# Kernel tuning notes

Hardware: AMD Instinct MI355X
Metric: run time of the kernel (lower is better)

Reference implementation:

```python
import jax, jax.numpy as jnp
import numpy as np
import math

EPS = 1.1920929e-07  # torch F.rms_norm default eps = fp32 machine epsilon


def rms_norm(x):
    # normalize over last dim, no learned weight (matches F.rms_norm(x, (d,)))
    var = jnp.mean(jnp.square(x), axis=-1, keepdims=True)
    return x * jax.lax.rsqrt(var + EPS)


def rotary(x, cos, sin):
    # x: (B, T, H, D); cos/sin: (T, D) -> broadcast over B, H
    d2 = x.shape[-1] // 2
    x1, x2 = x[..., :d2], x[..., d2:]
    rot = jnp.concatenate([-x2, x1], axis=-1)  # rotate_half
    c = cos[None, :, None, :]
    s = sin[None, :, None, :]
    return x * c + rot * s


def setup_inputs() -> dict:
    key = jax.random.key(0)
    ks = jax.random.split(key, 5)
    B, T, C, H = 2, 2048, 1024, 16
    D = C // H
    x = jax.random.normal(ks[0], (B, T, C), dtype=jnp.float32)
    # real RoPE tables (theta=10000), duplicated across the two halves
    inv_freq = 1.0 / (10000.0 ** (np.arange(0, D, 2, dtype=np.float32) / D))
    pos = np.arange(T, dtype=np.float32)
    freqs = np.outer(pos, inv_freq)            # (T, D/2)
    emb = np.concatenate([freqs, freqs], -1)   # (T, D)
    cos = jnp.asarray(np.cos(emb), dtype=jnp.float32)
    sin = jnp.asarray(np.sin(emb), dtype=jnp.float32)
    sc_in = 1.0 / math.sqrt(C)
    W_attn = jax.random.normal(ks[1], (C, 3 * C), dtype=jnp.float32) * sc_in
    b_attn = jax.random.normal(ks[2], (3 * C,), dtype=jnp.float32) * 0.02
    W_proj = jax.random.normal(ks[3], (C, C), dtype=jnp.float32) * sc_in
    b_proj = jax.random.normal(ks[4], (C,), dtype=jnp.float32) * 0.02
    return {"x": x, "cos": cos, "sin": sin, "W_attn": W_attn, "b_attn": b_attn,
            "W_proj": W_proj, "b_proj": b_proj}


def reference(x, cos, sin, W_attn, b_attn, W_proj, b_proj):
    B, T, C = x.shape
    H = 16
    D = C // H
    qkv = x @ W_attn + b_attn                         # (B, T, 3C)
    qkv = qkv.reshape(B, T, 3, H, D)                  # 'b t (a h d) -> ...'
    q, k, v = qkv[:, :, 0], qkv[:, :, 1], qkv[:, :, 2]  # (B, T, H, D)
    q, k = rms_norm(q), rms_norm(k)
    q = rotary(q, cos, sin)
    k = rotary(k, cos, sin)
    # causal SDPA, scale = 1/sqrt(D)
    scale = 1.0 / math.sqrt(D)
    scores = jnp.einsum('bthd,bshd->bhts', q, k) * scale  # (B, H, T, T)
    causal = jnp.tril(jnp.ones((T, T), dtype=bool))
    scores = jnp.where(causal[None, None], scores, jnp.finfo(scores.dtype).min)
    attn = jax.nn.softmax(scores, axis=-1)
    y = jnp.einsum('bhts,bshd->bthd', attn, v)            # (B, T, H, D)
    y = y.reshape(B, T, C)
    return y @ W_proj + b_proj
```

## Files before the change

### kernel.cpp

```cpp
#include <hip/hip_runtime.h>
#include <math.h>

#define EPSV 1.1920929e-07f

typedef __attribute__((ext_vector_type(8))) short short8;
typedef __attribute__((ext_vector_type(4))) float f32x4;

__device__ __forceinline__ float bf2f(unsigned short u) {
    union { unsigned int i; float f; } c; c.i = ((unsigned int)u) << 16; return c.f;
}
__device__ __forceinline__ unsigned short f2bf(float f) {
    union { float f; unsigned int i; } c; c.f = f;
    unsigned int r = c.i + 0x7FFFu + ((c.i >> 16) & 1u);
    return (unsigned short)(r >> 16);
}
__device__ __forceinline__ unsigned int pack_bf16_ru(float a, float b) {
    union { float f; unsigned int i; } ca, cb; ca.f = a; cb.f = b;
    return __builtin_amdgcn_perm(cb.i + 0x8000u, ca.i + 0x8000u, 0x07060302u);
}
__device__ __forceinline__ void async_lds16(const unsigned short* g, unsigned short* l) {
    __builtin_amdgcn_global_load_lds(
        (const __attribute__((address_space(1))) unsigned int*)g,
        (__attribute__((address_space(3))) unsigned int*)l, 16, 0, 0);
}

__global__ __launch_bounds__(256) void prep_cast_transpose(
    const float* __restrict__ x, unsigned short* __restrict__ xb, int nCast,
    const float* __restrict__ Wa, unsigned short* __restrict__ Wat,
    const float* __restrict__ Wp, unsigned short* __restrict__ Wpt,
    const float* __restrict__ cosp, const float* __restrict__ sinp,
    float2* __restrict__ cs, int castBlocks)
{
    __shared__ float tile[32][33];
    const int bxg = blockIdx.x;
    if (bxg < castBlocks) {
        const int i = (bxg * 256 + threadIdx.x) * 4;
        if (i >= nCast) return;
        const float4 v = *(const float4*)&x[i];
        ushort4 o;
        o.x = f2bf(v.x); o.y = f2bf(v.y); o.z = f2bf(v.z); o.w = f2bf(v.w);
        *(ushort4*)&xb[i] = o;
        return;
    }
    if (bxg >= castBlocks + 4096) {
        const int i = (bxg - castBlocks - 4096) * 256 + threadIdx.x;
        const int tp = i >> 5, dp = i & 31;
        cs[i] = make_float2(cosp[tp * 64 + dp], sinp[tp * 64 + dp]);
        return;
    }
    const int r0 = bxg - castBlocks;
    int bx = r0 & 127;
    const int by = r0 >> 7;
    const float* W; unsigned short* Wt; int N;
    if (bx < 96) { W = Wa; Wt = Wat; N = 3072; }
    else         { W = Wp; Wt = Wpt; N = 1024; bx -= 96; }
    const int n0 = bx * 32, k0 = by * 32;
    const int r = threadIdx.x >> 3, c4 = (threadIdx.x & 7) * 4;
    const float4 v = *(const float4*)&W[(size_t)(k0 + r) * N + n0 + c4];
    tile[r][c4 + 0] = v.x; tile[r][c4 + 1] = v.y;
    tile[r][c4 + 2] = v.z; tile[r][c4 + 3] = v.w;
    __syncthreads();
    ushort4 o;
    o.x = f2bf(tile[c4 + 0][r]); o.y = f2bf(tile[c4 + 1][r]);
    o.z = f2bf(tile[c4 + 2][r]); o.w = f2bf(tile[c4 + 3][r]);
    *(ushort4*)&Wt[(size_t)(n0 + r) * 1024 + k0 + c4] = o;
}

__global__ __launch_bounds__(256) void gemm_qkv(
    const unsigned short* __restrict__ A,
    const unsigned short* __restrict__ Bt,
    const float* __restrict__ bias,
    unsigned short* __restrict__ qkv,
    unsigned short* __restrict__ vt,
    const float2* __restrict__ cs,
    int M, int K, int T)
{
    const int N = 3072;
    __shared__ __align__(16) unsigned short smem[17408];
    unsigned short* As0 = smem;
    unsigned short* As1 = smem + 4096;
    unsigned short* Bs0 = smem + 8192;
    unsigned short* Bs1 = smem + 12288;

    const int t    = threadIdx.x;
    const int lane = t & 63;
    const int wv   = t >> 6;
    const int wrow = (wv >> 1) * 64;
    const int wcol = (wv & 1) * 64;
    const int m0 = blockIdx.y * 128;
    const int n0 = blockIdx.x * 128;
    const int col  = lane & 15;
    const int quad = lane >> 4;

    const int srow = (wv << 5) + (lane >> 2);
    const int scol = (lane & 3) << 3;
    const unsigned short* a00 = A  + (size_t)(m0 + srow) * K + scol;
    const unsigned short* a10 = a00 + (size_t)16 * K;
    const unsigned short* a01 = a00 + 32;
    const unsigned short* a11 = a10 + 32;
    const unsigned short* b00 = Bt + (size_t)(n0 + srow) * K + scol;
    const unsigned short* b10 = b00 + (size_t)16 * K;
    const unsigned short* b01 = b00 + 32;
    const unsigned short* b11 = b10 + 32;
    unsigned short* al0 = &As0[srow * 32 + scol];
    unsigned short* al1 = &As0[(srow + 16) * 32 + scol];
    unsigned short* al2 = &As1[srow * 32 + scol];
    unsigned short* al3 = &As1[(srow + 16) * 32 + scol];
    unsigned short* bl0 = &Bs0[srow * 32 + scol];
    unsigned short* bl1 = &Bs0[(srow + 16) * 32 + scol];
    unsigned short* bl2 = &Bs1[srow * 32 + scol];
    unsigned short* bl3 = &Bs1[(srow + 16) * 32 + scol];

    f32x4 acc[4][4];
    #pragma unroll
    for (int i = 0; i < 4; ++i)
        #pragma unroll
        for (int j = 0; j < 4; ++j)
            acc[i][j] = (f32x4){0.f, 0.f, 0.f, 0.f};

    for (int k0 = 0; k0 < K; k0 += 64) {
        async_lds16(a00, al0);
        async_lds16(a10, al1);
        async_lds16(a01, al2);
        async_lds16(a11, al3);
        async_lds16(b00, bl0);
        async_lds16(b10, bl1);
        async_lds16(b01, bl2);
        async_lds16(b11, bl3);
        a00 += 64; a10 += 64; a01 += 64; a11 += 64;
        b00 += 64; b10 += 64; b01 += 64; b11 += 64;
        __syncthreads();
        short8 af[2][4], bf[2][4];
        #pragma unroll
        for (int mt = 0; mt < 4; ++mt) {
            af[0][mt] = *(const short8*)&As0[(wrow + mt * 16 + col) * 32 + (quad << 3)];
            af[1][mt] = *(const short8*)&As1[(wrow + mt * 16 + col) * 32 + (quad << 3)];
        }
        #pragma unroll
        for (int nt = 0; nt < 4; ++nt) {
            bf[0][nt] = *(const short8*)&Bs0[(wcol + nt * 16 + col) * 32 + (quad << 3)];
            bf[1][nt] = *(const short8*)&Bs1[(wcol + nt * 16 + col) * 32 + (quad << 3)];
        }
        #pragma unroll
        for (int ks = 0; ks < 2; ++ks)
            #pragma unroll
            for (int mt = 0; mt < 4; ++mt)
                #pragma unroll
                for (int nt = 0; nt < 4; ++nt)
                    acc[mt][nt] = __builtin_amdgcn_mfma_f32_16x16x32_bf16(
                        af[ks][mt], bf[ks][nt], acc[mt][nt], 0, 0, 0);
        __syncthreads();
    }

    #pragma unroll
    for (int nt = 0; nt < 4; ++nt) {
        const float bv = bias[n0 + wcol + nt * 16 + col];
        #pragma unroll
        for (int mt = 0; mt < 4; ++mt)
            #pragma unroll
            for (int r = 0; r < 4; ++r)
                acc[mt][nt][r] += bv;
    }

    const int b     = m0 / T;
    const int tpos0 = m0 - b * T;

    if (n0 < 2048) {
        const int n_lin = n0 + wcol;
        const float scale = (n_lin < 1024) ? 0.18033688011112042f : 1.0f;
        #pragma unroll
        for (int mt = 0; mt < 4; ++mt) {
            #pragma unroll
            for (int r = 0; r < 4; ++r) {
                float ss = acc[mt][0][r] * acc[mt][0][r]
                         + acc[mt][1][r] * acc[mt][1][r]
                         + acc[mt][2][r] * acc[mt][2][r]
                         + acc[mt][3][r] * acc[mt][3][r];
                ss += __shfl_xor(ss, 1, 64);
                ss += __shfl_xor(ss, 2, 64);
                ss += __shfl_xor(ss, 4, 64);
                ss += __shfl_xor(ss, 8, 64);
                const float rn = rsqrtf(ss * (1.0f / 64.0f) + EPSV) * scale;
                const int tpos = tpos0 + wrow + mt * 16 + (quad << 2) + r;
                const float2 c0 = cs[tpos * 32 + col];
                const float2 c1 = cs[tpos * 32 + 16 + col];
                const float o0 = (acc[mt][0][r] * c0.x - acc[mt][2][r] * c0.y) * rn;
                const float o1 = (acc[mt][1][r] * c1.x - acc[mt][3][r] * c1.y) * rn;
                const float o2 = (acc[mt][2][r] * c0.x + acc[mt][0][r] * c0.y) * rn;
                const float o3 = (acc[mt][3][r] * c1.x + acc[mt][1][r] * c1.y) * rn;
                const int m = m0 + wrow + mt * 16 + (quad << 2) + r;
                unsigned short* qr = qkv + (size_t)m * N + n_lin + col;
                qr[0]  = f2bf(o0);
                qr[16] = f2bf(o1);
                qr[32] = f2bf(o2);
                qr[48] = f2bf(o3);
            }
        }
    } else {
        unsigned short (*vtile)[136] = (unsigned short(*)[136])smem;
        __syncthreads();
        #pragma unroll
        for (int nt = 0; nt < 4; ++nt)
            #pragma unroll
            for (int mt = 0; mt < 4; ++mt)
                #pragma unroll
                for (int r = 0; r < 4; ++r)
                    vtile[wcol + nt * 16 + col][wrow + mt * 16 + (quad << 2) + r]
                        = f2bf(acc[mt][nt][r]);
        __syncthreads();
        const int td = t >> 4;
        const int mloc = (t & 15) << 3;
        const int h2base = (n0 - 2048) >> 6;
        #pragma unroll
        for (int i = 0; i < 8; ++i) {
            const int dl = td + i * 16;
            const short8 o = *(const short8*)&vtile[dl][mloc];
            const int h2 = h2base + (dl >> 6);
            const size_t row = ((size_t)(b * 16 + h2) << 6) + (dl & 63);
            *(short8*)&vt[row * T + tpos0 + mloc] = o;
        }
    }
}

__global__ __launch_bounds__(256) void gemm_bf16_n64(
    const unsigned short* __restrict__ A,
    const unsigned short* __restrict__ Bt,
    const float* __restrict__ bias,
    float* __restrict__ C,
    int M, int N, int K)
{
    __shared__ unsigned short As0[128][32], As1[128][32];
    __shared__ unsigned short Bs0[64][32], Bs1[64][32];
    const int t    = threadIdx.x;
    const int lane = t & 63;
    const int wv   = t >> 6;
    const int wrow = wv << 5;
    const int m0 = blockIdx.y * 128;
    const int n0 = blockIdx.x * 64;
    const int col  = lane & 15;
    const int quad = lane >> 4;

    const int srow = (wv << 5) + (lane >> 2);
    const int scol = (lane & 3) << 3;
    const unsigned short* a00 = A  + (size_t)(m0 + srow) * K + scol;
    const unsigned short* a10 = a00 + (size_t)16 * K;
    const unsigned short* a01 = a00 + 32;
    const unsigned short* a11 = a10 + 32;
    const int bsrow = (wv << 4) + (lane >> 2);
    const unsigned short* b00 = Bt + (size_t)(n0 + bsrow) * K + scol;
    const unsigned short* b01 = b00 + 32;
    unsigned short* al0 = &As0[srow][scol];
    unsigned short* al1 = &As0[srow + 16][scol];
    unsigned short* al2 = &As1[srow][scol];
    unsigned short* al3 = &As1[srow + 16][scol];
    unsigned short* bl0 = &Bs0[bsrow][scol];
    unsigned short* bl1 = &Bs1[bsrow][scol];

    f32x4 acc[2][4];
    #pragma unroll
    for (int i = 0; i < 2; ++i)
        #pragma unroll
        for (int j = 0; j < 4; ++j)
            acc[i][j] = (f32x4){0.f, 0.f, 0.f, 0.f};

    for (int k0 = 0; k0 < K; k0 += 64) {
        async_lds16(a00, al0);
        async_lds16(a10, al1);
        async_lds16(a01, al2);
        async_lds16(a11, al3);
        async_lds16(b00, bl0);
        async_lds16(b01, bl1);
        a00 += 64; a10 += 64; a01 += 64; a11 += 64;
        b00 += 64; b01 += 64;
        __syncthreads();
        short8 af[2][2], bf[2][4];
        #pragma unroll
        for (int mt = 0; mt < 2; ++mt) {
            af[0][mt] = *(const short8*)&As0[wrow + mt * 16 + col][quad << 3];
            af[1][mt] = *(const short8*)&As1[wrow + mt * 16 + col][quad << 3];
        }
        #pragma unroll
        for (int nt = 0; nt < 4; ++nt) {
            bf[0][nt] = *(const short8*)&Bs0[nt * 16 + col][quad << 3];
            bf[1][nt] = *(const short8*)&Bs1[nt * 16 + col][quad << 3];
        }
        #pragma unroll
        for (int ks = 0; ks < 2; ++ks)
            #pragma unroll
            for (int mt = 0; mt < 2; ++mt)
                #pragma unroll
                for (int nt = 0; nt < 4; ++nt)
                    acc[mt][nt] = __builtin_amdgcn_mfma_f32_16x16x32_bf16(
                        af[ks][mt], bf[ks][nt], acc[mt][nt], 0, 0, 0);
        __syncthreads();
    }

    const int rowq = quad << 2;
    #pragma unroll
    for (int nt = 0; nt < 4; ++nt) {
        const int n = n0 + nt * 16 + col;
        const float bv = bias[n];
        #pragma unroll
        for (int mt = 0; mt < 2; ++mt) {
            #pragma unroll
            for (int r = 0; r < 4; ++r) {
                const int m = m0 + wrow + mt * 16 + rowq + r;
                C[(size_t)m * N + n] = acc[mt][nt][r] + bv;
            }
        }
    }
}

__global__ __launch_bounds__(512, 4) void flash_attn_mfma(
    const unsigned short* __restrict__ qkv,
    const unsigned short* __restrict__ vt,
    unsigned short* __restrict__ yb,
    int B, int T)
{
    const int bh = blockIdx.x;
    const int b  = bh >> 4, h = bh & 15;
    const int ny = (int)gridDim.y;
    const int y  = (int)blockIdx.y;
    const int hny = (ny + 1) >> 1;
    const int jq = (y < hny) ? (ny - 1 - y) : (y - hny);
    const int q0 = jq << 7;
    const int t  = threadIdx.x;
    const int lane = t & 63;
    const int w    = t >> 6;
    const int col  = lane & 15;
    const int quad = lane >> 4;

    __shared__ __align__(16) unsigned short smem[25600];
    unsigned short* Kb = smem;
    unsigned short* Vb = smem + 8192;
    unsigned short* Ps = smem + 16384;

    const unsigned short* qb  = qkv + (size_t)b * T * 3072 + (h << 6);
    const unsigned short* kb  = qb + 1024;
    const unsigned short* vtb = vt + (size_t)bh * 64 * T;

    const int qw = q0 + (w << 4);
    const int qg = qw + col;

    short8 qf[2];
    {
        const unsigned short* qrow = qb + (size_t)qg * 3072 + (quad << 3);
        qf[0] = *(const short8*)&qrow[0];
        qf[1] = *(const short8*)&qrow[32];
    }

    f32x4 oacc[4];
    #pragma unroll
    for (int i = 0; i < 4; ++i) oacc[i] = (f32x4){0.f, 0.f, 0.f, 0.f};
    float l_i = 0.f;

    const int sr = t >> 3;
    const int sg = (((t & 7) ^ (sr & 7)) << 3);
    const unsigned short* kp = kb  + (size_t)sr * 3072 + sg;
    const unsigned short* vp = vtb + (size_t)sr * T + sg;

    async_lds16(kp, Kb + (t << 3));
    async_lds16(vp, Vb + (t << 3));
    kp += (size_t)64 * 3072; vp += 64;

    const int cs0 = ((quad ^ (col & 7)) << 3);
    const int cs1 = (((4 + quad) ^ (col & 7)) << 3);

    const int last_kt = (q0 + 127) >> 6;
    int cur = 0;
    for (int kt = 0; kt <= last_kt; ++kt) {
        const int k0 = kt << 6;
        __syncthreads();
        if (kt < last_kt) {
            async_lds16(kp, Kb + ((cur ^ 1) << 12) + (t << 3));
            async_lds16(vp, Vb + ((cur ^ 1) << 12) + (t << 3));
            kp += (size_t)64 * 3072; vp += 64;
        }

        if (k0 <= qw + 15) {
            const unsigned short* Kc = Kb + (cur << 12);
            const unsigned short* Vc = Vb + (cur << 12);

            f32x4 st[4];
            #pragma unroll
            for (int i = 0; i < 4; ++i) st[i] = (f32x4){0.f, 0.f, 0.f, 0.f};
            __builtin_amdgcn_s_setprio(1);
            #pragma unroll
            for (int ks = 0; ks < 2; ++ks)
                #pragma unroll
                for (int mt = 0; mt < 4; ++mt) {
                    const short8 kf = *(const short8*)&Kc[(mt * 16 + col) * 64 + (ks ? cs1 : cs0)];
                    st[mt] = __builtin_amdgcn_mfma_f32_16x16x32_bf16(kf, qf[ks], st[mt], 0, 0, 0);
                }
            __builtin_amdgcn_s_setprio(0);

            const bool diag = (k0 + 63 > qw);
            unsigned short* pw = Ps + ((w << 4) + col) * 72;
            float rs = 0.f;
            #pragma unroll
            for (int mt = 0; mt < 4; ++mt) {
                float x0 = st[mt][0], x1 = st[mt][1];
                float x2 = st[mt][2], x3 = st[mt][3];
                if (diag) {
                    const int sbase = k0 + mt * 16 + (quad << 2);
                    if (sbase + 0 > qg) x0 = -INFINITY;
                    if (sbase + 1 > qg) x1 = -INFINITY;
                    if (sbase + 2 > qg) x2 = -INFINITY;
                    if (sbase + 3 > qg) x3 = -INFINITY;
                }
                const float p0 = __builtin_amdgcn_exp2f(x0);
                const float p1 = __builtin_amdgcn_exp2f(x1);
                const float p2 = __builtin_amdgcn_exp2f(x2);
                const float p3 = __builtin_amdgcn_exp2f(x3);
                rs += (p0 + p1) + (p2 + p3);
                uint2 pk;
                pk.x = pack_bf16_ru(p0, p1);
                pk.y = pack_bf16_ru(p2, p3);
                *(uint2*)&pw[mt * 16 + (quad << 2)] = pk;
            }
            l_i += rs;

            __builtin_amdgcn_s_setprio(1);
            #pragma unroll
            for (int ks = 0; ks < 2; ++ks) {
                const short8 pf = *(const short8*)&Ps[((w << 4) + col) * 72 + ks * 32 + (quad << 3)];
                #pragma unroll
                for (int mt = 0; mt < 4; ++mt) {
                    const short8 vf = *(const short8*)&Vc[(mt * 16 + col) * 64 + (ks ? cs1 : cs0)];
                    oacc[mt] = __builtin_amdgcn_mfma_f32_16x16x32_bf16(vf, pf, oacc[mt], 0, 0, 0);
                }
            }
            __builtin_amdgcn_s_setprio(0);
        }
        cur ^= 1;
    }

    l_i += __shfl_xor(l_i, 16, 64);
    l_i += __shfl_xor(l_i, 32, 64);
    const float inv = 1.0f / l_i;
    unsigned short* yrow = yb + (size_t)(b * T + qg) * 1024 + (h << 6);
    #pragma unroll
    for (int mt = 0; mt < 4; ++mt) {
        ushort4 yv;
        yv.x = f2bf(oacc[mt][0] * inv);
        yv.y = f2bf(oacc[mt][1] * inv);
        yv.z = f2bf(oacc[mt][2] * inv);
        yv.w = f2bf(oacc[mt][3] * inv);
        *(ushort4*)&yrow[mt * 16 + (quad << 2)] = yv;
    }
}

extern "C" void kernel_launch(void* const* d_in, const int* in_sizes, int n_in,
                              void* d_out, int out_size, void* d_ws, size_t ws_size,
                              hipStream_t stream)
{
    const float* x      = (const float*)d_in[0];
    const float* cosp   = (const float*)d_in[1];
    const float* sinp   = (const float*)d_in[2];
    const float* W_attn = (const float*)d_in[3];
    const float* b_attn = (const float*)d_in[4];
    const float* W_proj = (const float*)d_in[5];
    const float* b_proj = (const float*)d_in[6];
    float* out = (float*)d_out;

    const int C = 1024, H = 16;
    const int T  = in_sizes[1] / 64;
    const int BT = in_sizes[0] / C;
    const int B  = BT / T;

    float2* csb          = (float2*)d_ws;
    unsigned short* qkvb = (unsigned short*)(csb + (size_t)T * 32);
    unsigned short* xb   = qkvb + (size_t)BT * 3072;
    unsigned short* Wab  = xb   + (size_t)BT * 1024;
    unsigned short* Wpb  = Wab  + (size_t)3072 * 1024;
    unsigned short* yb   = Wpb  + (size_t)1024 * 1024;
    unsigned short* vtb  = yb   + (size_t)BT * 1024;

    const int castBlocks = BT * C / 1024;
    const int csBlocks   = T * 32 / 256;
    prep_cast_transpose<<<dim3(castBlocks + 4096 + csBlocks), dim3(256), 0, stream>>>(
        x, xb, BT * C, W_attn, Wab, W_proj, Wpb, cosp, sinp, csb, castBlocks);

    gemm_qkv<<<dim3(3 * C / 128, BT / 128), dim3(256), 0, stream>>>(
        xb, Wab, b_attn, qkvb, vtb, csb, BT, C, T);

    flash_attn_mfma<<<dim3(B * H, T / 128), dim3(512), 0, stream>>>(
        qkvb, vtb, yb, B, T);

    gemm_bf16_n64<<<dim3(C / 64, BT / 128), dim3(256), 0, stream>>>(
        yb, Wpb, b_proj, out, BT, C, C);
}
```

Measured before the change: 176.9 us.

## Double-buffer K=32 tiles with prefetch in QKV and projection GEMMs

Both bf16 GEMM kernels now load 32-wide K tiles into two alternating LDS buffers. The next tile is fetched asynchronously right after a single barrier, while the current tile is being consumed by MFMAs. This replaces the previous scheme, where each 64-wide K tile was loaded, then two barriers were issued per step with no overlap. The aim is to hide global-to-LDS load latency behind compute. In exchange there are more loop iterations with smaller tiles, and overlap still depends on where the compiler places the wait before each barrier.

```diff
diff --git a/kernel.cpp b/kernel.cpp
--- a/kernel.cpp
+++ b/kernel.cpp
@@ -77,10 +77,6 @@
 {
     const int N = 3072;
     __shared__ __align__(16) unsigned short smem[17408];
-    unsigned short* As0 = smem;
-    unsigned short* As1 = smem + 4096;
-    unsigned short* Bs0 = smem + 8192;
-    unsigned short* Bs1 = smem + 12288;
 
     const int t    = threadIdx.x;
     const int lane = t & 63;
@@ -92,24 +88,15 @@
     const int col  = lane & 15;
     const int quad = lane >> 4;
 
-    const int srow = (wv << 5) + (lane >> 2);
-    const int scol = (lane & 3) << 3;
-    const unsigned short* a00 = A  + (size_t)(m0 + srow) * K + scol;
-    const unsigned short* a10 = a00 + (size_t)16 * K;
-    const unsigned short* a01 = a00 + 32;
-    const unsigned short* a11 = a10 + 32;
-    const unsigned short* b00 = Bt + (size_t)(n0 + srow) * K + scol;
-    const unsigned short* b10 = b00 + (size_t)16 * K;
-    const unsigned short* b01 = b00 + 32;
-    const unsigned short* b11 = b10 + 32;
-    unsigned short* al0 = &As0[srow * 32 + scol];
-    unsigned short* al1 = &As0[(srow + 16) * 32 + scol];
-    unsigned short* al2 = &As1[srow * 32 + scol];
-    unsigned short* al3 = &As1[(srow + 16) * 32 + scol];
-    unsigned short* bl0 = &Bs0[srow * 32 + scol];
-    unsigned short* bl1 = &Bs0[(srow + 16) * 32 + scol];
-    unsigned short* bl2 = &Bs1[srow * 32 + scol];
-    unsigned short* bl3 = &Bs1[(srow + 16) * 32 + scol];
+    const int srw = lane >> 2;
+    const int sck = (lane & 3) << 3;
+    const unsigned short* aP0 = A  + (size_t)(m0 + (wv << 4) + srw) * K + sck;
+    const unsigned short* aP1 = aP0 + (size_t)64 * K;
+    const unsigned short* bP0 = Bt + (size_t)(n0 + (wv << 4) + srw) * K + sck;
+    const unsigned short* bP1 = bP0 + (size_t)64 * K;
+    const int stoff = (wv << 9) + (lane << 3);
+    unsigned short* aD = smem + stoff;
+    unsigned short* bD = smem + 8192 + stoff;
 
     f32x4 acc[4][4];
     #pragma unroll
@@ -118,38 +105,34 @@
         for (int j = 0; j < 4; ++j)
             acc[i][j] = (f32x4){0.f, 0.f, 0.f, 0.f};
 
-    for (int k0 = 0; k0 < K; k0 += 64) {
-        async_lds16(a00, al0);
-        async_lds16(a10, al1);
-        async_lds16(a01, al2);
-        async_lds16(a11, al3);
-        async_lds16(b00, bl0);
-        async_lds16(b10, bl1);
-        async_lds16(b01, bl2);
-        async_lds16(b11, bl3);
-        a00 += 64; a10 += 64; a01 += 64; a11 += 64;
-        b00 += 64; b10 += 64; b01 += 64; b11 += 64;
+    async_lds16(aP0, aD);        async_lds16(aP1, aD + 2048);
+    async_lds16(bP0, bD);        async_lds16(bP1, bD + 2048);
+    aP0 += 32; aP1 += 32; bP0 += 32; bP1 += 32;
+
+    const int NK = K >> 5;
+    for (int kt = 0; kt < NK; ++kt) {
         __syncthreads();
-        short8 af[2][4], bf[2][4];
-        #pragma unroll
-        for (int mt = 0; mt < 4; ++mt) {
-            af[0][mt] = *(const short8*)&As0[(wrow + mt * 16 + col) * 32 + (quad << 3)];
-            af[1][mt] = *(const short8*)&As1[(wrow + mt * 16 + col) * 32 + (quad << 3)];
-        }
-        #pragma unroll
-        for (int nt = 0; nt < 4; ++nt) {
-            bf[0][nt] = *(const short8*)&Bs0[(wcol + nt * 16 + col) * 32 + (quad << 3)];
-            bf[1][nt] = *(const short8*)&Bs1[(wcol + nt * 16 + col) * 32 + (quad << 3)];
-        }
-        #pragma unroll
-        for (int ks = 0; ks < 2; ++ks)
-            #pragma unroll
-            for (int mt = 0; mt < 4; ++mt)
-                #pragma unroll
-                for (int nt = 0; nt < 4; ++nt)
-                    acc[mt][nt] = __builtin_amdgcn_mfma_f32_16x16x32_bf16(
-                        af[ks][mt], bf[ks][nt], acc[mt][nt], 0, 0, 0);
-        __syncthreads();
+        if (kt + 1 < NK) {
+            const int nb = ((kt + 1) & 1) << 12;
+            async_lds16(aP0, aD + nb);  async_lds16(aP1, aD + nb + 2048);
+            async_lds16(bP0, bD + nb);  async_lds16(bP1, bD + nb + 2048);
+            aP0 += 32; aP1 += 32; bP0 += 32; bP1 += 32;
+        }
+        const unsigned short* Ac = smem + ((kt & 1) << 12);
+        const unsigned short* Bc = smem + 8192 + ((kt & 1) << 12);
+        short8 af[4], bf[4];
+        #pragma unroll
+        for (int mt = 0; mt < 4; ++mt)
+            af[mt] = *(const short8*)&Ac[(wrow + mt * 16 + col) * 32 + (quad << 3)];
+        #pragma unroll
+        for (int nt = 0; nt < 4; ++nt)
+            bf[nt] = *(const short8*)&Bc[(wcol + nt * 16 + col) * 32 + (quad << 3)];
+        #pragma unroll
+        for (int mt = 0; mt < 4; ++mt)
+            #pragma unroll
+            for (int nt = 0; nt < 4; ++nt)
+                acc[mt][nt] = __builtin_amdgcn_mfma_f32_16x16x32_bf16(
+                    af[mt], bf[nt], acc[mt][nt], 0, 0, 0);
     }
 
     #pragma unroll
@@ -229,8 +212,7 @@
     float* __restrict__ C,
     int M, int N, int K)
 {
-    __shared__ unsigned short As0[128][32], As1[128][32];
-    __shared__ unsigned short Bs0[64][32], Bs1[64][32];
+    __shared__ __align__(16) unsigned short smem[12288];
     const int t    = threadIdx.x;
     const int lane = t & 63;
     const int wv   = t >> 6;
@@ -240,21 +222,14 @@
     const int col  = lane & 15;
     const int quad = lane >> 4;
 
-    const int srow = (wv << 5) + (lane >> 2);
-    const int scol = (lane & 3) << 3;
-    const unsigned short* a00 = A  + (size_t)(m0 + srow) * K + scol;
-    const unsigned short* a10 = a00 + (size_t)16 * K;
-    const unsigned short* a01 = a00 + 32;
-    const unsigned short* a11 = a10 + 32;
-    const int bsrow = (wv << 4) + (lane >> 2);
-    const unsigned short* b00 = Bt + (size_t)(n0 + bsrow) * K + scol;
-    const unsigned short* b01 = b00 + 32;
-    unsigned short* al0 = &As0[srow][scol];
-    unsigned short* al1 = &As0[srow + 16][scol];
-    unsigned short* al2 = &As1[srow][scol];
-    unsigned short* al3 = &As1[srow + 16][scol];
-    unsigned short* bl0 = &Bs0[bsrow][scol];
-    unsigned short* bl1 = &Bs1[bsrow][scol];
+    const int srw = lane >> 2;
+    const int sck = (lane & 3) << 3;
+    const unsigned short* aP0 = A  + (size_t)(m0 + (wv << 4) + srw) * K + sck;
+    const unsigned short* aP1 = aP0 + (size_t)64 * K;
+    const unsigned short* bP0 = Bt + (size_t)(n0 + (wv << 4) + srw) * K + sck;
+    const int stoff = (wv << 9) + (lane << 3);
+    unsigned short* aD = smem + stoff;
+    unsigned short* bD = smem + 8192 + stoff;
 
     f32x4 acc[2][4];
     #pragma unroll
@@ -263,36 +238,35 @@
         for (int j = 0; j < 4; ++j)
             acc[i][j] = (f32x4){0.f, 0.f, 0.f, 0.f};
 
-    for (int k0 = 0; k0 < K; k0 += 64) {
-        async_lds16(a00, al0);
-        async_lds16(a10, al1);
-        async_lds16(a01, al2);
-        async_lds16(a11, al3);
-        async_lds16(b00, bl0);
-        async_lds16(b01, bl1);
-        a00 += 64; a10 += 64; a01 += 64; a11 += 64;
-        b00 += 64; b01 += 64;
+    async_lds16(aP0, aD);  async_lds16(aP1, aD + 2048);
+    async_lds16(bP0, bD);
+    aP0 += 32; aP1 += 32; bP0 += 32;
+
+    const int NK = K >> 5;
+    for (int kt = 0; kt < NK; ++kt) {
         __syncthreads();
-        short8 af[2][2], bf[2][4];
-        #pragma unroll
-        for (int mt = 0; mt < 2; ++mt) {
-            af[0][mt] = *(const short8*)&As0[wrow + mt * 16 + col][quad << 3];
-            af[1][mt] = *(const short8*)&As1[wrow + mt * 16 + col][quad << 3];
-        }
-        #pragma unroll
-        for (int nt = 0; nt < 4; ++nt) {
-            bf[0][nt] = *(const short8*)&Bs0[nt * 16 + col][quad << 3];
-            bf[1][nt] = *(const short8*)&Bs1[nt * 16 + col][quad << 3];
-        }
-        #pragma unroll
-        for (int ks = 0; ks < 2; ++ks)
-            #pragma unroll
-            for (int mt = 0; mt < 2; ++mt)
-                #pragma unroll
-                for (int nt = 0; nt < 4; ++nt)
-                    acc[mt][nt] = __builtin_amdgcn_mfma_f32_16x16x32_bf16(
-                        af[ks][mt], bf[ks][nt], acc[mt][nt], 0, 0, 0);
-        __syncthreads();
+        if (kt + 1 < NK) {
+            const int nbA = ((kt + 1) & 1) << 12;
+            const int nbB = ((kt + 1) & 1) << 11;
+            async_lds16(aP0, aD + nbA);  async_lds16(aP1, aD + nbA + 2048);
+            async_lds16(bP0, bD + nbB);
+            aP0 += 32; aP1 += 32; bP0 += 32;
+        }
+        const unsigned short* Ac = smem + ((kt & 1) << 12);
+        const unsigned short* Bc = smem + 8192 + ((kt & 1) << 11);
+        short8 af[2], bf[4];
+        #pragma unroll
+        for (int mt = 0; mt < 2; ++mt)
+            af[mt] = *(const short8*)&Ac[(wrow + mt * 16 + col) * 32 + (quad << 3)];
+        #pragma unroll
+        for (int nt = 0; nt < 4; ++nt)
+            bf[nt] = *(const short8*)&Bc[(nt * 16 + col) * 32 + (quad << 3)];
+        #pragma unroll
+        for (int mt = 0; mt < 2; ++mt)
+            #pragma unroll
+            for (int nt = 0; nt < 4; ++nt)
+                acc[mt][nt] = __builtin_amdgcn_mfma_f32_16x16x32_bf16(
+                    af[mt], bf[nt], acc[mt][nt], 0, 0, 0);
     }
 
     const int rowq = quad << 2;
```

New measurement: 174.0 us. No clear change (-1.6%).
